# Optimization experiments

Hardware: AMD Instinct MI355X
Metric: run time of the kernel (lower is better)

Reference implementation:

```python
import jax, jax.numpy as jnp
import numpy as np

N_DATA = 500000
EMB = 256
K = 4096
BS = 64
T = 0.07
M = 0.5


def _l2norm(x, axis=-1, eps=1e-12):
    return x / jnp.maximum(jnp.linalg.norm(x, axis=axis, keepdims=True), eps)


def setup_inputs() -> dict:
    key = jax.random.key(0)
    k1, k2, k3, k4, k5, k6 = jax.random.split(key, 6)
    vis_feat = jax.random.normal(k1, (BS, EMB), dtype=jnp.float32)
    text_feat = jax.random.normal(k2, (BS, EMB), dtype=jnp.float32)
    # memory banks: original inits uniform in [-stdv, stdv]; randn scaled works the same numerically
    stdv = 1.0 / np.sqrt(EMB / 3)
    vis_memory = jax.random.uniform(k3, (N_DATA, EMB), dtype=jnp.float32, minval=-stdv, maxval=stdv)
    text_memory = jax.random.uniform(k4, (N_DATA, EMB), dtype=jnp.float32, minval=-stdv, maxval=stdv)
    idx = jax.random.randint(k5, (BS,), 0, N_DATA, dtype=jnp.int32)
    slct_idx = jax.random.randint(k6, (BS, K + 1), 0, N_DATA, dtype=jnp.int32)
    # column 0 holds the positive index, as in slct_idx.select(1,0).copy_(idx)
    slct_idx = slct_idx.at[:, 0].set(idx)
    return {
        "vis_feat": vis_feat,
        "text_feat": text_feat,
        "vis_memory": vis_memory,
        "text_memory": text_memory,
        "slct_idx": slct_idx,
        "idx": idx,
    }


def reference(vis_feat, text_feat, vis_memory, text_memory, slct_idx, idx):
    # embeddings are L2-normalized before use (nn.functional.normalize(dim=1))
    vn = _l2norm(vis_feat)   # [bs, D]
    tn = _l2norm(text_feat)  # [bs, D]

    # gather K+1 negatives/positive from memory banks (detached in original)
    tf = jax.lax.stop_gradient(text_memory[slct_idx])  # [bs, K+1, D]
    vf = jax.lax.stop_gradient(vis_memory[slct_idx])   # [bs, K+1, D]

    # batched dot products + exp(./T) (bmm with [bs, D, 1])
    vis_out = jnp.exp(jnp.einsum("bkd,bd->bk", tf, vn) / T)   # [bs, K+1]
    text_out = jnp.exp(jnp.einsum("bkd,bd->bk", vf, tn) / T)  # [bs, K+1]

    # NCE normalization constants, set on first pass: Z = mean * N_data
    Z_v = jax.lax.stop_gradient(jnp.mean(vis_out)) * N_DATA
    Z_t = jax.lax.stop_gradient(jnp.mean(text_out)) * N_DATA
    vis_out = vis_out / Z_v
    text_out = text_out / Z_t

    # EMA memory update + renormalize + scatter (no_grad in original)
    vis_pos = vis_memory[idx] * M + jax.lax.stop_gradient(vn) * (1.0 - M)
    text_pos = text_memory[idx] * M + jax.lax.stop_gradient(tn) * (1.0 - M)
    new_vis_memory = vis_memory.at[idx].set(_l2norm(vis_pos))
    new_text_memory = text_memory.at[idx].set(_l2norm(text_pos))

    return vis_out, text_out, new_vis_memory, new_text_memory
```

## Files before the change

### kernel.cpp

```cpp
#include <hip/hip_runtime.h>

#define NDATA 500000
#define EMB   256
#define BS    64
#define KP1   4097
#define NPAIR (BS * KP1)
#define INV_T (1.0f / 0.07f)

#define SCAN_EPB 2048
#define NB_SCAN  ((NDATA + SCAN_EPB - 1) / SCAN_EPB)
#define NBLK     2048
#define NBY      17

__global__ __launch_bounds__(256) void normalize_kernel(
    const float* __restrict__ vis_feat, const float* __restrict__ text_feat,
    float* __restrict__ vn, float* __restrict__ tn) {
  int b = blockIdx.x & 63;
  bool is_vis = blockIdx.x < 64;
  const float* src = (is_vis ? vis_feat : text_feat) + b * EMB;
  float* dst = (is_vis ? vn : tn) + b * EMB;
  int t = threadIdx.x;
  float x = src[t];
  float s = x * x;
  for (int off = 32; off > 0; off >>= 1) s += __shfl_down(s, off, 64);
  __shared__ float red[4];
  if ((t & 63) == 0) red[t >> 6] = s;
  __syncthreads();
  float norm = sqrtf(red[0] + red[1] + red[2] + red[3]);
  dst[t] = x / fmaxf(norm, 1e-12f);
}

__global__ __launch_bounds__(256) void build_counts_kernel(
    const int* __restrict__ slct, unsigned* __restrict__ counts,
    unsigned* __restrict__ old) {
  int i = blockIdx.x * 256 + threadIdx.x;
  if (i < NPAIR) {
    int r = slct[i];
    old[i] = atomicAdd(&counts[r], 1u);
  }
}

__global__ __launch_bounds__(256) void scan1_kernel(
    const unsigned* __restrict__ counts, unsigned* __restrict__ start,
    unsigned* __restrict__ bsum) {
  int t = threadIdx.x;
  int base = blockIdx.x * SCAN_EPB + t * 8;
  unsigned v[8];
  unsigned tsum = 0;
#pragma unroll
  for (int j = 0; j < 8; ++j) {
    int i = base + j;
    unsigned c = (i < NDATA) ? counts[i] : 0u;
    v[j] = tsum;
    tsum += c;
  }
  unsigned x = tsum;
  for (int d = 1; d < 64; d <<= 1) {
    unsigned y = __shfl_up(x, d, 64);
    if ((t & 63) >= d) x += y;
  }
  __shared__ unsigned wsum[4];
  if ((t & 63) == 63) wsum[t >> 6] = x;
  __syncthreads();
  unsigned woff = 0;
  for (int wv = 0; wv < (t >> 6); ++wv) woff += wsum[wv];
  unsigned ex = woff + x - tsum;
#pragma unroll
  for (int j = 0; j < 8; ++j) {
    int i = base + j;
    if (i < NDATA) start[i] = ex + v[j];
  }
  if (t == 255) bsum[blockIdx.x] = woff + x;
}

__global__ __launch_bounds__(256) void scan2_kernel(unsigned* __restrict__ bsum) {
  int t = threadIdx.x;
  unsigned v = (t < NB_SCAN) ? bsum[t] : 0u;
  unsigned x = v;
  for (int d = 1; d < 64; d <<= 1) {
    unsigned y = __shfl_up(x, d, 64);
    if ((t & 63) >= d) x += y;
  }
  __shared__ unsigned wsum[4];
  if ((t & 63) == 63) wsum[t >> 6] = x;
  __syncthreads();
  unsigned woff = 0;
  for (int wv = 0; wv < (t >> 6); ++wv) woff += wsum[wv];
  unsigned ex = woff + x - v;
  if (t < NB_SCAN) bsum[t] = ex;
}

__global__ __launch_bounds__(256) void scatter_kernel(
    const int* __restrict__ slct, const unsigned* __restrict__ start,
    const unsigned* __restrict__ bsum, const unsigned* __restrict__ old,
    unsigned* __restrict__ pairs) {
  int i = blockIdx.x * 256 + threadIdx.x;
  if (i < NPAIR) {
    int r = slct[i];
    unsigned pos = start[r] + bsum[r >> 11] + old[i];
    pairs[pos] = (unsigned)i;
  }
}

__global__ __launch_bounds__(256) void fused_copy_dot_kernel(
    const float* __restrict__ text_mem, const float* __restrict__ vis_mem,
    float* __restrict__ out_text, float* __restrict__ out_vis,
    const float* __restrict__ vn, const float* __restrict__ tn,
    const unsigned* __restrict__ counts, const unsigned* __restrict__ start,
    const unsigned* __restrict__ bsum, const unsigned* __restrict__ pairs,
    float* __restrict__ out, float* __restrict__ partials) {
  int z = blockIdx.z;
  const float4* s4 = (const float4*)(z == 0 ? text_mem : vis_mem);
  float4* d4 = (float4*)(z == 0 ? out_text : out_vis);
  const float4* f4 = (const float4*)(z == 0 ? vn : tn);
  float* outz = out + (size_t)z * NPAIR;

  int t = threadIdx.x, w = t >> 6, lane = t & 63;
  const int nwaves = NBLK * 4;
  const int rpw = (NDATA + nwaves - 1) / nwaves;
  int gw = blockIdx.x * 4 + w;
  int r0 = gw * rpw;
  int rend = min(r0 + rpw, NDATA);

  float local = 0.f;
  if (r0 < rend) {
    float4 v = s4[(size_t)r0 * 64 + lane];
    for (int r = r0; r < rend; ++r) {
      float4 vnext = make_float4(0.f, 0.f, 0.f, 0.f);
      if (r + 1 < rend) vnext = s4[(size_t)(r + 1) * 64 + lane];
      d4[(size_t)r * 64 + lane] = v;
      unsigned nref = counts[r];
      if (nref) {
        unsigned gs = start[r] + bsum[r >> 11];
        for (unsigned j = 0; j < nref; ++j) {
          unsigned i = pairs[gs + j];
          int b = (int)(i / KP1);
          float4 fv = f4[b * 64 + lane];
          float p = v.x * fv.x + v.y * fv.y + v.z * fv.z + v.w * fv.w;
          for (int off = 32; off > 0; off >>= 1) p += __shfl_down(p, off, 64);
          if (lane == 0) {
            float e = __expf(p * INV_T);
            outz[i] = e;
            local += e;
          }
        }
      }
      v = vnext;
    }
  }
  __shared__ float red[4];
  if (lane == 0) red[w] = local;
  __syncthreads();
  if (t == 0)
    partials[(size_t)z * NBLK + blockIdx.x] = red[0] + red[1] + red[2] + red[3];
}

__global__ __launch_bounds__(256) void reduce_z_kernel(
    const float* __restrict__ partials, float* __restrict__ zsum, int per_z) {
  int z = blockIdx.x;
  const float* p = partials + (size_t)z * per_z;
  float s = 0.f;
  for (int i = threadIdx.x; i < per_z; i += 256) s += p[i];
  for (int off = 32; off > 0; off >>= 1) s += __shfl_down(s, off, 64);
  __shared__ float red[4];
  if ((threadIdx.x & 63) == 0) red[threadIdx.x >> 6] = s;
  __syncthreads();
  if (threadIdx.x == 0) zsum[z] = red[0] + red[1] + red[2] + red[3];
}

__global__ __launch_bounds__(256) void scale_kernel(
    float* __restrict__ out, const float* __restrict__ zsum) {
  const float c = (float)NDATA / (float)NPAIR;
  int i = blockIdx.x * blockDim.x + threadIdx.x;
  const int n = 2 * NPAIR;
  if (i < n) {
    float Z = ((i < NPAIR) ? zsum[0] : zsum[1]) * c;
    out[i] = out[i] / Z;
  }
}

__global__ __launch_bounds__(256) void update_kernel(
    const float* __restrict__ vis_mem, const float* __restrict__ text_mem,
    const float* __restrict__ vn, const float* __restrict__ tn,
    const int* __restrict__ idx,
    float* __restrict__ out_vis, float* __restrict__ out_text) {
  int b = blockIdx.x & 63;
  bool is_vis = blockIdx.x < 64;
  int row = idx[b];
  for (int b2 = b + 1; b2 < BS; ++b2)
    if (idx[b2] == row) return;
  const float* mem  = (is_vis ? vis_mem : text_mem) + (size_t)row * EMB;
  const float* feat = (is_vis ? vn : tn) + b * EMB;
  float* dst = (is_vis ? out_vis : out_text) + (size_t)row * EMB;
  int t = threadIdx.x;
  float p = mem[t] * 0.5f + feat[t] * 0.5f;
  float s = p * p;
  for (int off = 32; off > 0; off >>= 1) s += __shfl_down(s, off, 64);
  __shared__ float red[4];
  if ((t & 63) == 0) red[t >> 6] = s;
  __syncthreads();
  float norm = sqrtf(red[0] + red[1] + red[2] + red[3]);
  dst[t] = p / fmaxf(norm, 1e-12f);
}

__global__ __launch_bounds__(256) void dot_exp_kernel(
    const float* __restrict__ text_mem, const float* __restrict__ vis_mem,
    const float* __restrict__ vn, const float* __restrict__ tn,
    const int* __restrict__ slct, float* __restrict__ out,
    float* __restrict__ partials) {
  int b = blockIdx.x;
  int z = blockIdx.z;
  const float* mem  = (z == 0) ? text_mem : vis_mem;
  const float* feat = (z == 0) ? vn : tn;
  float* o = out + (size_t)z * NPAIR + (size_t)b * KP1;
  const int* srow = slct + b * KP1;
  __shared__ float4 sf[64];
  int t = threadIdx.x;
  if (t < 64) sf[t] = ((const float4*)(feat + b * EMB))[t];
  __syncthreads();
  int w = t >> 6, lane = t & 63;
  float4 f = sf[lane];
  int kbase = blockIdx.y * 256 + w * 64;
  int kend  = min(kbase + 64, KP1);
  float local = 0.f;
  int k = kbase;
  for (; k + 2 <= kend; k += 2) {
    int r0 = srow[k], r1 = srow[k + 1];
    float4 v0 = ((const float4*)(mem + (size_t)r0 * EMB))[lane];
    float4 v1 = ((const float4*)(mem + (size_t)r1 * EMB))[lane];
    float p0 = v0.x * f.x + v0.y * f.y + v0.z * f.z + v0.w * f.w;
    float p1 = v1.x * f.x + v1.y * f.y + v1.z * f.z + v1.w * f.w;
    for (int off = 32; off > 0; off >>= 1) {
      p0 += __shfl_down(p0, off, 64);
      p1 += __shfl_down(p1, off, 64);
    }
    if (lane == 0) {
      float e0 = __expf(p0 * INV_T);
      float e1 = __expf(p1 * INV_T);
      o[k] = e0; o[k + 1] = e1;
      local += e0 + e1;
    }
  }
  if (k < kend) {
    int r0 = srow[k];
    float4 v0 = ((const float4*)(mem + (size_t)r0 * EMB))[lane];
    float p0 = v0.x * f.x + v0.y * f.y + v0.z * f.z + v0.w * f.w;
    for (int off = 32; off > 0; off >>= 1) p0 += __shfl_down(p0, off, 64);
    if (lane == 0) { float e0 = __expf(p0 * INV_T); o[k] = e0; local += e0; }
  }
  __shared__ float red[4];
  if (lane == 0) red[w] = local;
  __syncthreads();
  if (t == 0)
    partials[((size_t)z * NBY + blockIdx.y) * BS + b] =
        red[0] + red[1] + red[2] + red[3];
}

__global__ __launch_bounds__(256) void copy2_kernel(
    const float4* __restrict__ src_a, float4* __restrict__ dst_a,
    const float4* __restrict__ src_b, float4* __restrict__ dst_b, long n4) {
  long i = (long)blockIdx.x * blockDim.x + threadIdx.x;
  long stride = (long)gridDim.x * blockDim.x;
  for (; i < 2 * n4; i += stride) {
    if (i < n4) dst_a[i] = src_a[i];
    else        dst_b[i - n4] = src_b[i - n4];
  }
}

extern "C" void kernel_launch(void* const* d_in, const int* in_sizes, int n_in,
                              void* d_out, int out_size, void* d_ws, size_t ws_size,
                              hipStream_t stream) {
  const float* vis_feat  = (const float*)d_in[0];
  const float* text_feat = (const float*)d_in[1];
  const float* vis_mem   = (const float*)d_in[2];
  const float* text_mem  = (const float*)d_in[3];
  const int*   slct      = (const int*)d_in[4];
  const int*   idx       = (const int*)d_in[5];

  float* out          = (float*)d_out;
  float* out_vis_mem  = out + (size_t)2 * NPAIR;
  float* out_text_mem = out_vis_mem + (size_t)NDATA * EMB;

  float* ws   = (float*)d_ws;
  float*    vn       = ws;
  float*    tn       = vn + BS * EMB;
  float*    zsum     = tn + BS * EMB;
  float*    partials = zsum + 2;
  unsigned* counts   = (unsigned*)(partials + 2 * NBLK);
  unsigned* start    = counts + NDATA;
  unsigned* bsum     = start + NDATA;
  unsigned* old      = bsum + 256;
  unsigned* pairs    = old + NPAIR;
  size_t needed = ((size_t)(2 * BS * EMB + 2 + 2 * NBLK) +
                   (size_t)(2 * NDATA + 256 + 2 * NPAIR)) * 4;

  normalize_kernel<<<128, 256, 0, stream>>>(vis_feat, text_feat, vn, tn);

  if (ws_size >= needed) {
    hipMemsetAsync(counts, 0, NDATA * sizeof(unsigned), stream);
    build_counts_kernel<<<(NPAIR + 255) / 256, 256, 0, stream>>>(slct, counts, old);
    scan1_kernel<<<NB_SCAN, 256, 0, stream>>>(counts, start, bsum);
    scan2_kernel<<<1, 256, 0, stream>>>(bsum);
    scatter_kernel<<<(NPAIR + 255) / 256, 256, 0, stream>>>(slct, start, bsum, old, pairs);

    dim3 gF(NBLK, 1, 2);
    fused_copy_dot_kernel<<<gF, 256, 0, stream>>>(
        text_mem, vis_mem, out_text_mem, out_vis_mem, vn, tn,
        counts, start, bsum, pairs, out, partials);

    reduce_z_kernel<<<2, 256, 0, stream>>>(partials, zsum, NBLK);
  } else {
    dim3 gB(BS, NBY, 2);
    dot_exp_kernel<<<gB, 256, 0, stream>>>(text_mem, vis_mem, vn, tn, slct, out,
                                           partials);
    reduce_z_kernel<<<2, 256, 0, stream>>>(partials, zsum, NBY * BS);
    const long n4 = (long)NDATA * EMB / 4;
    copy2_kernel<<<8192, 256, 0, stream>>>(
        (const float4*)vis_mem,  (float4*)out_vis_mem,
        (const float4*)text_mem, (float4*)out_text_mem, n4);
  }

  scale_kernel<<<(2 * NPAIR + 255) / 256, 256, 0, stream>>>(out, zsum);

  update_kernel<<<128, 256, 0, stream>>>(vis_mem, text_mem, vn, tn, idx,
                                         out_vis_mem, out_text_mem);
}
```

Measured before the change: 491.0 us.

## Batch row copies with nontemporal double-buffered loads and merge small kernels

The fused copy-plus-dot kernel now gives each wave 64 rows and processes them in chunks of 8. The next chunk is prefetched into a second register buffer, and loads and stores use nontemporal builtins. Counts and start offsets are read as vectors, and pair entries are packed as (batch<<13 | k) so the per-reference integer division goes away. Normalization is merged with the histogram kernel and scaling with the memory update, which removes two launches. The cost is higher register use from the 16 float4 buffers and longer, more complex code.

```diff
diff --git a/kernel.cpp b/kernel.cpp
--- a/kernel.cpp
+++ b/kernel.cpp
@@ -9,34 +9,40 @@
 
 #define SCAN_EPB 2048
 #define NB_SCAN  ((NDATA + SCAN_EPB - 1) / SCAN_EPB)
-#define NBLK     2048
+#define RPW      64
+#define NBLKF    ((NDATA + RPW * 4 - 1) / (RPW * 4))
+#define SCALE_BLKS ((2 * NPAIR + 255) / 256)
 #define NBY      17
 
-__global__ __launch_bounds__(256) void normalize_kernel(
+typedef float    f32x4 __attribute__((ext_vector_type(4)));
+typedef unsigned u32x4 __attribute__((ext_vector_type(4)));
+
+__global__ __launch_bounds__(256) void norm_hist_kernel(
     const float* __restrict__ vis_feat, const float* __restrict__ text_feat,
-    float* __restrict__ vn, float* __restrict__ tn) {
-  int b = blockIdx.x & 63;
-  bool is_vis = blockIdx.x < 64;
-  const float* src = (is_vis ? vis_feat : text_feat) + b * EMB;
-  float* dst = (is_vis ? vn : tn) + b * EMB;
-  int t = threadIdx.x;
-  float x = src[t];
-  float s = x * x;
-  for (int off = 32; off > 0; off >>= 1) s += __shfl_down(s, off, 64);
-  __shared__ float red[4];
-  if ((t & 63) == 0) red[t >> 6] = s;
-  __syncthreads();
-  float norm = sqrtf(red[0] + red[1] + red[2] + red[3]);
-  dst[t] = x / fmaxf(norm, 1e-12f);
-}
-
-__global__ __launch_bounds__(256) void build_counts_kernel(
+    float* __restrict__ vn, float* __restrict__ tn,
     const int* __restrict__ slct, unsigned* __restrict__ counts,
     unsigned* __restrict__ old) {
-  int i = blockIdx.x * 256 + threadIdx.x;
-  if (i < NPAIR) {
-    int r = slct[i];
-    old[i] = atomicAdd(&counts[r], 1u);
+  int bid = blockIdx.x;
+  if (bid < 128) {
+    int b = bid & 63;
+    bool is_vis = bid < 64;
+    const float* src = (is_vis ? vis_feat : text_feat) + b * EMB;
+    float* dst = (is_vis ? vn : tn) + b * EMB;
+    int t = threadIdx.x;
+    float x = src[t];
+    float s = x * x;
+    for (int off = 32; off > 0; off >>= 1) s += __shfl_down(s, off, 64);
+    __shared__ float red[4];
+    if ((t & 63) == 0) red[t >> 6] = s;
+    __syncthreads();
+    float norm = sqrtf(red[0] + red[1] + red[2] + red[3]);
+    dst[t] = x / fmaxf(norm, 1e-12f);
+  } else {
+    int i = (bid - 128) * 256 + threadIdx.x;
+    if (i < NPAIR) {
+      int r = slct[i];
+      old[i] = atomicAdd(&counts[r], 1u);
+    }
   }
 }
 
@@ -98,9 +104,45 @@
   if (i < NPAIR) {
     int r = slct[i];
     unsigned pos = start[r] + bsum[r >> 11] + old[i];
-    pairs[pos] = (unsigned)i;
-  }
-}
+    int b = i / KP1;
+    int kk = i - b * KP1;
+    pairs[pos] = ((unsigned)b << 13) | (unsigned)kk;
+  }
+}
+
+#define LOADC(R, rb)                                                          \
+  { _Pragma("unroll") for (int j = 0; j < 8; ++j)                             \
+      R[j] = __builtin_nontemporal_load(&s4[(size_t)((rb) + j) * 64 + lane]); }
+
+#define STOREC(R, rb)                                                         \
+  { _Pragma("unroll") for (int j = 0; j < 8; ++j)                             \
+      __builtin_nontemporal_store(R[j], &d4[(size_t)((rb) + j) * 64 + lane]); }
+
+#define REFS(R, rb)                                                           \
+  { u32x4 c0 = *(const u32x4*)&counts[(rb)];                                  \
+    u32x4 c1 = *(const u32x4*)&counts[(rb) + 4];                              \
+    u32x4 s0 = *(const u32x4*)&start[(rb)];                                   \
+    u32x4 s1 = *(const u32x4*)&start[(rb) + 4];                               \
+    unsigned cn[8] = {c0.x, c0.y, c0.z, c0.w, c1.x, c1.y, c1.z, c1.w};        \
+    unsigned sn[8] = {s0.x, s0.y, s0.z, s0.w, s1.x, s1.y, s1.z, s1.w};        \
+    _Pragma("unroll") for (int j = 0; j < 8; ++j) {                           \
+      unsigned n = cn[j];                                                     \
+      if (n) {                                                                \
+        unsigned gs = sn[j] + bs;                                             \
+        for (unsigned u = 0; u < n; ++u) {                                    \
+          unsigned p = pairs[gs + u];                                         \
+          int bb = (int)(p >> 13), kk = (int)(p & 8191u);                     \
+          f32x4 fv = f4[bb * 64 + lane];                                      \
+          float d = R[j].x * fv.x + R[j].y * fv.y + R[j].z * fv.z + R[j].w * fv.w; \
+          for (int off = 32; off > 0; off >>= 1) d += __shfl_down(d, off, 64);\
+          if (lane == 0) {                                                    \
+            float e = __expf(d * INV_T);                                      \
+            outz[bb * KP1 + kk] = e;                                          \
+            local += e;                                                       \
+          }                                                                   \
+        }                                                                     \
+      }                                                                       \
+    } }
 
 __global__ __launch_bounds__(256) void fused_copy_dot_kernel(
     const float* __restrict__ text_mem, const float* __restrict__ vis_mem,
@@ -110,49 +152,39 @@
     const unsigned* __restrict__ bsum, const unsigned* __restrict__ pairs,
     float* __restrict__ out, float* __restrict__ partials) {
   int z = blockIdx.z;
-  const float4* s4 = (const float4*)(z == 0 ? text_mem : vis_mem);
-  float4* d4 = (float4*)(z == 0 ? out_text : out_vis);
-  const float4* f4 = (const float4*)(z == 0 ? vn : tn);
+  const f32x4* s4 = (const f32x4*)(z == 0 ? text_mem : vis_mem);
+  f32x4* d4 = (f32x4*)(z == 0 ? out_text : out_vis);
+  const f32x4* f4 = (const f32x4*)(z == 0 ? vn : tn);
   float* outz = out + (size_t)z * NPAIR;
 
   int t = threadIdx.x, w = t >> 6, lane = t & 63;
-  const int nwaves = NBLK * 4;
-  const int rpw = (NDATA + nwaves - 1) / nwaves;
   int gw = blockIdx.x * 4 + w;
-  int r0 = gw * rpw;
-  int rend = min(r0 + rpw, NDATA);
-
+  int r0 = gw * RPW;
   float local = 0.f;
-  if (r0 < rend) {
-    float4 v = s4[(size_t)r0 * 64 + lane];
-    for (int r = r0; r < rend; ++r) {
-      float4 vnext = make_float4(0.f, 0.f, 0.f, 0.f);
-      if (r + 1 < rend) vnext = s4[(size_t)(r + 1) * 64 + lane];
-      d4[(size_t)r * 64 + lane] = v;
-      unsigned nref = counts[r];
-      if (nref) {
-        unsigned gs = start[r] + bsum[r >> 11];
-        for (unsigned j = 0; j < nref; ++j) {
-          unsigned i = pairs[gs + j];
-          int b = (int)(i / KP1);
-          float4 fv = f4[b * 64 + lane];
-          float p = v.x * fv.x + v.y * fv.y + v.z * fv.z + v.w * fv.w;
-          for (int off = 32; off > 0; off >>= 1) p += __shfl_down(p, off, 64);
-          if (lane == 0) {
-            float e = __expf(p * INV_T);
-            outz[i] = e;
-            local += e;
-          }
-        }
-      }
-      v = vnext;
+
+  if (r0 < NDATA) {
+    int rend = min(r0 + RPW, NDATA);
+    int nch = (rend - r0) >> 3;
+    unsigned bs = bsum[r0 >> 11];
+    f32x4 A[8], B[8];
+    int rb = r0, c = 0;
+    LOADC(A, rb);
+    while (true) {
+      if (c + 1 < nch) LOADC(B, rb + 8);
+      STOREC(A, rb);
+      REFS(A, rb);
+      ++c; rb += 8; if (c >= nch) break;
+      if (c + 1 < nch) LOADC(A, rb + 8);
+      STOREC(B, rb);
+      REFS(B, rb);
+      ++c; rb += 8; if (c >= nch) break;
     }
   }
   __shared__ float red[4];
   if (lane == 0) red[w] = local;
   __syncthreads();
   if (t == 0)
-    partials[(size_t)z * NBLK + blockIdx.x] = red[0] + red[1] + red[2] + red[3];
+    partials[(size_t)z * NBLKF + blockIdx.x] = red[0] + red[1] + red[2] + red[3];
 }
 
 __global__ __launch_bounds__(256) void reduce_z_kernel(
@@ -168,39 +200,39 @@
   if (threadIdx.x == 0) zsum[z] = red[0] + red[1] + red[2] + red[3];
 }
 
-__global__ __launch_bounds__(256) void scale_kernel(
-    float* __restrict__ out, const float* __restrict__ zsum) {
-  const float c = (float)NDATA / (float)NPAIR;
-  int i = blockIdx.x * blockDim.x + threadIdx.x;
-  const int n = 2 * NPAIR;
-  if (i < n) {
-    float Z = ((i < NPAIR) ? zsum[0] : zsum[1]) * c;
-    out[i] = out[i] / Z;
-  }
-}
-
-__global__ __launch_bounds__(256) void update_kernel(
+__global__ __launch_bounds__(256) void scale_update_kernel(
+    float* __restrict__ out, const float* __restrict__ zsum,
     const float* __restrict__ vis_mem, const float* __restrict__ text_mem,
     const float* __restrict__ vn, const float* __restrict__ tn,
     const int* __restrict__ idx,
     float* __restrict__ out_vis, float* __restrict__ out_text) {
-  int b = blockIdx.x & 63;
-  bool is_vis = blockIdx.x < 64;
-  int row = idx[b];
-  for (int b2 = b + 1; b2 < BS; ++b2)
-    if (idx[b2] == row) return;
-  const float* mem  = (is_vis ? vis_mem : text_mem) + (size_t)row * EMB;
-  const float* feat = (is_vis ? vn : tn) + b * EMB;
-  float* dst = (is_vis ? out_vis : out_text) + (size_t)row * EMB;
-  int t = threadIdx.x;
-  float p = mem[t] * 0.5f + feat[t] * 0.5f;
-  float s = p * p;
-  for (int off = 32; off > 0; off >>= 1) s += __shfl_down(s, off, 64);
-  __shared__ float red[4];
-  if ((t & 63) == 0) red[t >> 6] = s;
-  __syncthreads();
-  float norm = sqrtf(red[0] + red[1] + red[2] + red[3]);
-  dst[t] = p / fmaxf(norm, 1e-12f);
+  int bid = blockIdx.x;
+  if (bid < SCALE_BLKS) {
+    int i = bid * 256 + threadIdx.x;
+    if (i < 2 * NPAIR) {
+      float Z = ((i < NPAIR) ? zsum[0] : zsum[1]) * ((float)NDATA / (float)NPAIR);
+      out[i] = out[i] / Z;
+    }
+  } else {
+    int bb = bid - SCALE_BLKS;
+    int b = bb & 63;
+    bool is_vis = bb < 64;
+    int row = idx[b];
+    for (int b2 = b + 1; b2 < BS; ++b2)
+      if (idx[b2] == row) return;
+    const float* mem  = (is_vis ? vis_mem : text_mem) + (size_t)row * EMB;
+    const float* feat = (is_vis ? vn : tn) + b * EMB;
+    float* dst = (is_vis ? out_vis : out_text) + (size_t)row * EMB;
+    int t = threadIdx.x;
+    float p = mem[t] * 0.5f + feat[t] * 0.5f;
+    float s = p * p;
+    for (int off = 32; off > 0; off >>= 1) s += __shfl_down(s, off, 64);
+    __shared__ float red[4];
+    if ((t & 63) == 0) red[t >> 6] = s;
+    __syncthreads();
+    float norm = sqrtf(red[0] + red[1] + red[2] + red[3]);
+    dst[t] = p / fmaxf(norm, 1e-12f);
+  }
 }
 
 __global__ __launch_bounds__(256) void dot_exp_kernel(
@@ -281,35 +313,36 @@
   float* out_vis_mem  = out + (size_t)2 * NPAIR;
   float* out_text_mem = out_vis_mem + (size_t)NDATA * EMB;
 
-  float* ws   = (float*)d_ws;
+  float*    ws       = (float*)d_ws;
   float*    vn       = ws;
   float*    tn       = vn + BS * EMB;
   float*    zsum     = tn + BS * EMB;
-  float*    partials = zsum + 2;
-  unsigned* counts   = (unsigned*)(partials + 2 * NBLK);
+  float*    partials = zsum + 4;
+  unsigned* counts   = (unsigned*)(partials + 2 * NBLKF);
   unsigned* start    = counts + NDATA;
   unsigned* bsum     = start + NDATA;
   unsigned* old      = bsum + 256;
   unsigned* pairs    = old + NPAIR;
-  size_t needed = ((size_t)(2 * BS * EMB + 2 + 2 * NBLK) +
+  size_t needed = ((size_t)(2 * BS * EMB + 4 + 2 * NBLKF) +
                    (size_t)(2 * NDATA + 256 + 2 * NPAIR)) * 4;
-
-  normalize_kernel<<<128, 256, 0, stream>>>(vis_feat, text_feat, vn, tn);
 
   if (ws_size >= needed) {
     hipMemsetAsync(counts, 0, NDATA * sizeof(unsigned), stream);
-    build_counts_kernel<<<(NPAIR + 255) / 256, 256, 0, stream>>>(slct, counts, old);
+    norm_hist_kernel<<<128 + (NPAIR + 255) / 256, 256, 0, stream>>>(
+        vis_feat, text_feat, vn, tn, slct, counts, old);
     scan1_kernel<<<NB_SCAN, 256, 0, stream>>>(counts, start, bsum);
     scan2_kernel<<<1, 256, 0, stream>>>(bsum);
     scatter_kernel<<<(NPAIR + 255) / 256, 256, 0, stream>>>(slct, start, bsum, old, pairs);
 
-    dim3 gF(NBLK, 1, 2);
+    dim3 gF(NBLKF, 1, 2);
     fused_copy_dot_kernel<<<gF, 256, 0, stream>>>(
         text_mem, vis_mem, out_text_mem, out_vis_mem, vn, tn,
         counts, start, bsum, pairs, out, partials);
 
-    reduce_z_kernel<<<2, 256, 0, stream>>>(partials, zsum, NBLK);
+    reduce_z_kernel<<<2, 256, 0, stream>>>(partials, zsum, NBLKF);
   } else {
+    norm_hist_kernel<<<128, 256, 0, stream>>>(
+        vis_feat, text_feat, vn, tn, slct, counts, old);
     dim3 gB(BS, NBY, 2);
     dot_exp_kernel<<<gB, 256, 0, stream>>>(text_mem, vis_mem, vn, tn, slct, out,
                                            partials);
@@ -320,8 +353,6 @@
         (const float4*)text_mem, (float4*)out_text_mem, n4);
   }
 
-  scale_kernel<<<(2 * NPAIR + 255) / 256, 256, 0, stream>>>(out, zsum);
-
-  update_kernel<<<128, 256, 0, stream>>>(vis_mem, text_mem, vn, tn, idx,
-                                         out_vis_mem, out_text_mem);
-}
+  scale_update_kernel<<<SCALE_BLKS + 128, 256, 0, stream>>>(
+      out, zsum, vis_mem, text_mem, vn, tn, idx, out_vis_mem, out_text_mem);
+}
```

Measured after the change: 458.9 us. 1.07x faster.
